# Kernel optimization log

Measured on AMD Instinct MI355X. Metric: run time of the kernel, lower is better.

## Reference

```python
import jax, jax.numpy as jnp
import numpy as np

B = 512      # parcels (batch)
P = 128      # pois per parcel
N = B * P    # poi nodes
E = 524288   # intra-parcel poi-poi edges
IN = 64
H = 128
OUT = 16
IMG = 2048
HEADS = 3


def seg_mean(x, seg, n):
    s = jax.ops.segment_sum(x, seg, num_segments=n)
    c = jax.ops.segment_sum(jnp.ones((x.shape[0],), x.dtype), seg, num_segments=n)
    return s / c[:, None]


def segment_softmax(e, seg, n):
    m = jax.ops.segment_max(e, seg, num_segments=n)
    ex = jnp.exp(e - m[seg])
    s = jax.ops.segment_sum(ex, seg, num_segments=n)
    return ex / s[seg]


def gcn_layer(x, src, dst, n, W, b):
    # symmetric-normalized GCN with self loops over an edge list
    deg = jax.ops.segment_sum(jnp.ones((src.shape[0],), x.dtype), dst, num_segments=n) + 1.0
    norm = jax.lax.rsqrt(deg)
    h = x * norm[:, None]
    agg = jax.ops.segment_sum(h[src], dst, num_segments=n) + h  # self loop
    return (agg * norm[:, None]) @ W + b


def gat(h_src_in, h_dst_in, src, dst, n_dst, W, al, ar, bias):
    # DGL-style GATConv (shared fc for src/dst), heads=HEADS
    hs = (h_src_in @ W).reshape(-1, HEADS, H)
    hd = (h_dst_in @ W).reshape(-1, HEADS, H)
    el = (hs * al).sum(-1)  # [Ns, heads]
    er = (hd * ar).sum(-1)  # [Nd, heads]
    e = jax.nn.leaky_relu(el[src] + er[dst], 0.2)  # [E, heads]
    alpha = segment_softmax(e, dst, n_dst)
    out = jax.ops.segment_sum(alpha[:, :, None] * hs[src], dst, num_segments=n_dst)
    return out + bias.reshape(HEADS, H)


def setup_inputs() -> dict:
    key = jax.random.key(0)
    ks = jax.random.split(key, 30)
    rng = np.random.default_rng(0)
    src = rng.integers(0, N, size=E)
    dst = (src // P) * P + rng.integers(0, P, size=E)  # intra-parcel edges
    edges = jnp.asarray(np.stack([src, dst]), dtype=jnp.int32)
    segment_ids = jnp.asarray(np.arange(N) // P, dtype=jnp.int32)
    s = 0.05
    n = lambda k, shp: jax.random.normal(k, shp, jnp.float32) * s
    return {
        "poi_x": jax.random.normal(ks[0], (N, IN), jnp.float32),
        "img_feat": jax.random.normal(ks[1], (B, IMG), jnp.float32),
        "edges": edges,
        "segment_ids": segment_ids,
        "T0": 0.98,
        # poi_encoder 2-layer GCN
        "W1": n(ks[2], (IN, H)), "b1": jnp.zeros((H,)),
        "W2": n(ks[3], (H, H)), "b2": jnp.zeros((H,)),
        # hrs_encoder.fc (ResNet backbone replaced by precomputed [B,2048] feats)
        "Whrs": n(ks[4], (IMG, H)), "bhrs": jnp.zeros((H,)),
        # proj_hrs / proj_poi
        "Wph": n(ks[5], (H, H)), "bph": jnp.zeros((H,)),
        "Wpp": n(ks[6], (H, H)), "bpp": jnp.zeros((H,)),
        # GATConv 'in' (poi -> parcel) and 'with' (parcel -> poi)
        "Wg_in": n(ks[7], (H, HEADS * H)), "al_in": n(ks[8], (HEADS, H)), "ar_in": n(ks[9], (HEADS, H)), "bg_in": jnp.zeros((HEADS * H,)),
        "Wg_w": n(ks[10], (H, HEADS * H)), "al_w": n(ks[11], (HEADS, H)), "ar_w": n(ks[12], (HEADS, H)), "bg_w": jnp.zeros((HEADS * H,)),
        # VanillaGCN (1 layer) on parcel similarity graph
        "Wh1": n(ks[13], (H, H)), "bh1": jnp.zeros((H,)),
        "Wp1": n(ks[14], (H, H)), "bp1": jnp.zeros((H,)),
        # final fc (4*hid -> out)
        "Wfc": n(ks[15], (4 * H, OUT)), "bfc": jnp.zeros((OUT,)),
    }


def reference(poi_x, img_feat, edges, segment_ids, T0,
              W1, b1, W2, b2, Whrs, bhrs, Wph, bph, Wpp, bpp,
              Wg_in, al_in, ar_in, bg_in, Wg_w, al_w, ar_w, bg_w,
              Wh1, bh1, Wp1, bp1, Wfc, bfc):
    src, dst = edges[0], edges[1]
    # encoders
    hrs = img_feat @ Whrs + bhrs                                   # [B,H]
    h1 = jax.nn.relu(gcn_layer(poi_x, src, dst, N, W1, b1))
    poi_node = gcn_layer(h1, src, dst, N, W2, b2)                  # [N,H]
    ori_poi = poi_node
    poi_pool = seg_mean(poi_node, segment_ids, B)                  # dgl.mean_nodes
    # parcel similarity
    med_fused = jnp.concatenate([hrs, poi_pool], axis=1)
    med_fused = med_fused / jnp.linalg.norm(med_fused, axis=1, keepdims=True)
    med = (med_fused @ med_fused.T + 1.0) / 2.0                    # [B,B]
    # UniSimGraph: threshold -> dense parcel graph -> 1-layer GCNs
    adj = jnp.maximum(jnp.where(med >= T0, 1.0, 0.0), jnp.eye(B, dtype=med.dtype))
    dinv = jax.lax.rsqrt(adj.sum(1))
    A = dinv[:, None] * adj * dinv[None, :]
    hrs_agg = A @ hrs @ Wh1 + bh1
    poi_agg = A @ poi_pool @ Wp1 + bp1
    # getHetGraph: bipartite GATs between pois and their parcel
    ph = hrs @ Wph + bph
    pp = ori_poi @ Wpp + bpp
    poi_idx = jnp.arange(N, dtype=segment_ids.dtype)
    poi2img = gat(pp, ph, poi_idx, segment_ids, B, Wg_in, al_in, ar_in, bg_in).mean(1)  # parcel out
    img2poi = gat(ph, pp, segment_ids, poi_idx, N, Wg_w, al_w, ar_w, bg_w).mean(1)      # poi out
    img2poi = seg_mean(img2poi, segment_ids, B)
    # MutualAgg concat order: [img2poi, poi2poi, poi2img, img2img]
    agg = jnp.concatenate([img2poi, poi_agg, poi2img, hrs_agg], axis=1)  # [B,4H]
    out = agg @ Wfc + bfc
    return out, med
```

## Files before the change

kernel.cpp:

```cpp
#include <hip/hip_runtime.h>
#include <stdint.h>

#define NN 65536
#define EE 524288
#define BB 512

typedef unsigned short u16;
typedef __attribute__((ext_vector_type(8))) short s8v;
typedef __attribute__((ext_vector_type(4))) float f32x4;

__device__ __forceinline__ u16 f2b(float f) {
  union { float f; uint32_t u; } a{f};
  uint32_t r = a.u + 0x7fff + ((a.u >> 16) & 1);
  return (u16)(r >> 16);
}
__device__ __forceinline__ float b2f(u16 v) {
  union { uint32_t u; float f; } a{(uint32_t)v << 16};
  return a.f;
}
__device__ __forceinline__ int swz128(int r, int c) { return r * 128 + (c ^ ((r & 7) << 3)); }
__device__ __forceinline__ int swz64(int r, int c) { return r * 64 + (c ^ ((r & 7) << 3)); }

__global__ void __launch_bounds__(256) k_prep_graph(
    const int* __restrict__ src, const int* __restrict__ dst, uint32_t* __restrict__ Sg,
    const float* __restrict__ W1, const float* __restrict__ W2,
    const float* __restrict__ Wg_in, const float* __restrict__ al_in,
    const float* __restrict__ ar_in, const float* __restrict__ Wpp,
    const float* __restrict__ bpp, u16* __restrict__ w1t, u16* __restrict__ w2t,
    float* __restrict__ wv, float* __restrict__ q, float* __restrict__ ch,
    const float* __restrict__ Wg_w, const float* __restrict__ Wfc,
    const float* __restrict__ bph, const float* __restrict__ bg_in,
    float* __restrict__ B0, float* __restrict__ Ch, float* __restrict__ D0,
    float* __restrict__ Evec, int* __restrict__ rowcnt) {
  int blk = blockIdx.x, t = threadIdx.x;
  if (blk < 2048) {
    int e = blk * 256 + t;
    int s = src[e] & 127, d = dst[e];
    atomicAdd(&Sg[((size_t)d * 128 + s) >> 2], 1u << ((s & 3) * 8));
  } else if (blk < 2144) {
    int i = (blk - 2048) * 256 + t;
    if (i < 8192) {
      int n = i >> 6, k = i & 63;
      w1t[i] = f2b(W1[k * 128 + n]);
    } else {
      int j = i - 8192;
      int n = j >> 7, k = j & 127;
      w2t[j] = f2b(W2[k * 128 + n]);
    }
  } else if (blk == 2144) {
    __shared__ float su[384];
    for (int i = t; i < 384; i += 256) {
      int h = i >> 7, k = i & 127;
      float s = 0.f, sw = 0.f;
#pragma unroll 4
      for (int c = 0; c < 128; ++c) {
        float g = Wg_in[k * 384 + h * 128 + c];
        s += g * al_in[h * 128 + c];
        sw += g * ar_in[h * 128 + c];
      }
      su[i] = s;
      wv[i] = sw;
    }
    __syncthreads();
    for (int i = t; i < 384; i += 256) {
      int h = i >> 7, j = i & 127;
      float s = 0.f;
#pragma unroll 4
      for (int k = 0; k < 128; ++k) s += Wpp[j * 128 + k] * su[h * 128 + k];
      q[i] = s;
    }
    if (t < 3) {
      float s = 0.f;
#pragma unroll 4
      for (int k = 0; k < 128; ++k) s += bpp[k] * su[t * 128 + k];
      ch[t] = s;
    }
  } else if (blk < 2153) {
    int bb = blk - 2145;
    __shared__ float sW[2048];
    for (int i = t; i < 2048; i += 256) sW[i] = Wfc[i];
    __syncthreads();
    int m = bb * 16 + (t >> 4), o = t & 15;
    const float* wr = Wg_w + (size_t)m * 384;
    float acc = 0.f;
#pragma unroll 4
    for (int j = 0; j < 128; ++j) {
      float g = (wr[j] + wr[128 + j] + wr[256 + j]) * (1.0f / 3.0f);
      acc += g * sW[j * 16 + o];
    }
    B0[m * 16 + o] = acc;
  } else if (blk < 2177) {
    int bb = blk - 2153;
    int h = bb >> 3, rc = bb & 7;
    __shared__ float sW[2048];
    for (int i = t; i < 2048; i += 256) sW[i] = Wfc[256 * 16 + i];
    __syncthreads();
    int m = rc * 16 + (t >> 4), o = t & 15;
    const float* wr = Wg_in + (size_t)m * 384 + h * 128;
    float acc = 0.f;
#pragma unroll 4
    for (int c = 0; c < 128; ++c) acc += wr[c] * sW[c * 16 + o];
    Ch[((size_t)h * 128 + m) * 16 + o] = acc;
  } else if (blk == 2177) {
    __shared__ float sD[2][128];
    int j = t & 127, half = t >> 7;
    int k0 = half * 64;
    float acc = 0.f;
#pragma unroll 4
    for (int k = k0; k < k0 + 64; ++k) {
      float g = (Wg_w[k * 384 + j] + Wg_w[k * 384 + 128 + j] + Wg_w[k * 384 + 256 + j]) *
                (1.0f / 3.0f);
      acc += bph[k] * g;
    }
    sD[half][j] = acc;
    __syncthreads();
    if (t < 128) D0[t] = sD[0][t] + sD[1][t];
  } else if (blk == 2178) {
    __shared__ float sE[2][128];
    int j = t & 127, half = t >> 7;
    int m0 = half * 64;
    float e = 0.f;
    for (int h = 0; h < 3; ++h) {
#pragma unroll 4
      for (int m = m0; m < m0 + 64; ++m) e += bpp[m] * Wg_in[m * 384 + h * 128 + j];
    }
    sE[half][j] = e;
    __syncthreads();
    if (t < 128) {
      float g0in = (bg_in[t] + bg_in[128 + t] + bg_in[256 + t]) * (1.0f / 3.0f);
      Evec[t] = (sE[0][t] + sE[1][t]) * (1.0f / 3.0f) + g0in;
    }
  } else {
    if (t < 256) {
      rowcnt[t] = 0;
      rowcnt[t + 256] = 0;
    }
  }
}

__global__ void __launch_bounds__(256) k_fold2(
    const float* __restrict__ Wph, const float* __restrict__ Wh1,
    const float* __restrict__ Wp1, const float* __restrict__ Wpp,
    const float* __restrict__ Wfc, const float* __restrict__ bfc,
    const float* __restrict__ bh1, const float* __restrict__ bp1,
    const float* __restrict__ bg_w, const float* __restrict__ B0,
    const float* __restrict__ Ch, const float* __restrict__ D0,
    const float* __restrict__ Evec, float* __restrict__ Afold,
    float* __restrict__ bias_out) {
  int blk = blockIdx.x, t = threadIdx.x;
  if (blk < 48) {
    int mat = blk >> 3, rc = blk & 7;
    __shared__ float sW[2048];
    if (mat == 0)
      for (int i = t; i < 2048; i += 256) sW[i] = B0[i];
    else if (mat == 1)
      for (int i = t; i < 2048; i += 256) sW[i] = Wfc[384 * 16 + i];
    else if (mat == 2)
      for (int i = t; i < 2048; i += 256) sW[i] = Wfc[128 * 16 + i];
    else
      for (int i = t; i < 2048; i += 256) sW[i] = Ch[(size_t)(mat - 3) * 2048 + i];
    __syncthreads();
    int k = rc * 16 + (t >> 4), o = t & 15;
    const float* L = (mat == 0) ? Wph : (mat == 1) ? Wh1 : (mat == 2) ? Wp1 : Wpp;
    float scale = (mat >= 3) ? (1.0f / 3.0f) : 1.0f;
    const float* lr = L + (size_t)k * 128;
    float acc = 0.f;
#pragma unroll 4
    for (int m = 0; m < 128; ++m) acc += lr[m] * sW[m * 16 + o];
    Afold[(size_t)mat * 2048 + k * 16 + o] = acc * scale;
  } else {
    __shared__ float sRed[16][16];
    int o = t & 15, chunk = t >> 4;
    int j0 = chunk * 8;
    float acc = 0.f;
#pragma unroll
    for (int jj = 0; jj < 8; ++jj) {
      int j = j0 + jj;
      float g0w = (bg_w[j] + bg_w[128 + j] + bg_w[256 + j]) * (1.0f / 3.0f);
      acc += (D0[j] + g0w) * Wfc[j * 16 + o];
      acc += bp1[j] * Wfc[(128 + j) * 16 + o];
      acc += Evec[j] * Wfc[(256 + j) * 16 + o];
      acc += bh1[j] * Wfc[(384 + j) * 16 + o];
    }
    sRed[o][chunk] = acc;
    __syncthreads();
    if (t < 16) {
      float a = bfc[t];
#pragma unroll
      for (int c = 0; c < 16; ++c) a += sRed[t][c];
      bias_out[t] = a;
    }
  }
}

__global__ void __launch_bounds__(1024) k_hrs(const float* __restrict__ img,
                                              const float* __restrict__ Whrs,
                                              const float* __restrict__ bhrs,
                                              const float* __restrict__ Wph,
                                              const float* __restrict__ bph,
                                              const float* __restrict__ wv,
                                              float* __restrict__ hrs, float* __restrict__ er) {
  __shared__ float sI[4096];
  __shared__ float sRed[8][128];
  __shared__ float sHrs[2][128];
  __shared__ float sPh[2][128];
  int r0 = blockIdx.x * 2;
  int t = threadIdx.x;
  const float4* gsrc = (const float4*)(img + (size_t)r0 * 2048);
  float4* ldst = (float4*)sI;
  if (t < 1024) ldst[t] = gsrc[t];
  __syncthreads();
  int c = t & 127, g = t >> 7;
  int row = g & 1, ks = g >> 1;
  const float* s = sI + row * 2048 + ks * 512;
  const float* W = Whrs + (size_t)(ks * 512) * 128 + c;
  float a0 = 0.f, a1 = 0.f, a2 = 0.f, a3 = 0.f;
  for (int k = 0; k < 512; k += 4) {
    a0 += s[k] * W[(size_t)k * 128];
    a1 += s[k + 1] * W[(size_t)(k + 1) * 128];
    a2 += s[k + 2] * W[(size_t)(k + 2) * 128];
    a3 += s[k + 3] * W[(size_t)(k + 3) * 128];
  }
  sRed[g][c] = (a0 + a1) + (a2 + a3);
  __syncthreads();
  if (t < 256) {
    int rr = t >> 7, cc = t & 127;
    float v = sRed[rr][cc] + sRed[rr + 2][cc] + sRed[rr + 4][cc] + sRed[rr + 6][cc] + bhrs[cc];
    hrs[(r0 + rr) * 128 + cc] = v;
    sHrs[rr][cc] = v;
  }
  __syncthreads();
  if (t < 256) {
    int rr = t >> 7, cc = t & 127;
    float acc = bph[cc];
#pragma unroll 4
    for (int k = 0; k < 128; ++k) acc += sHrs[rr][k] * Wph[k * 128 + cc];
    sPh[rr][cc] = acc;
  }
  __syncthreads();
  if (t < 6) {
    int rr = t / 3, h = t % 3;
    float s2 = 0.f;
#pragma unroll 4
    for (int k = 0; k < 128; ++k) s2 += sPh[rr][k] * wv[h * 128 + k];
    er[(r0 + rr) * 3 + h] = s2;
  }
}

__global__ void __launch_bounds__(1024) k_gcn_fused(
    const float* __restrict__ x, const float* __restrict__ b1, const float* __restrict__ b2,
    const uint8_t* __restrict__ Sg8, const float* __restrict__ q, const float* __restrict__ ch,
    const float* __restrict__ er, const float* __restrict__ hrs,
    const u16* __restrict__ w1t, const u16* __restrict__ w2t, float* __restrict__ poi_pool,
    float* __restrict__ pooled, u16* __restrict__ mfnb) {
  extern __shared__ char sm[];
  u16* sS = (u16*)sm;
  u16* sB2 = (u16*)(sm + 32768);
  u16* sPt = (u16*)(sm + 32768);
  u16* sXt = (u16*)(sm + 65536);
  u16* sAgg1 = (u16*)(sm + 81920);
  u16* sW1t = (u16*)(sm + 98304);
  float* sXrm = (float*)(sm + 114688);
  u16* sW2t = (u16*)(sm + 114688);
  u16* sAgg2 = (u16*)(sm + 65536);
  u16* sP = (u16*)sm;
  float* sNorm = (float*)(sm + 147968);
  float* sQ = (float*)(sm + 148480);
  float* sAl = (float*)(sm + 150016);
  float* sPool = (float*)(sm + 151552);
  float* sEr = (float*)(sm + 152064);
  float* sCh = (float*)(sm + 152080);

  int b = blockIdx.x, t = threadIdx.x;
  int base = b << 7;
  int l = t & 63, w = t >> 6;
  int wm = w & 7, wn = w >> 3;
  const uint8_t* Sgb = Sg8 + (size_t)base * 128;

  int rown = t >> 3, q8 = t & 7;
  uint4 cw = *(const uint4*)(Sgb + rown * 128 + q8 * 16);
  {
    uint32_t words[4] = {cw.x, cw.y, cw.z, cw.w};
    uint32_t bs = 0;
#pragma unroll
    for (int p = 0; p < 4; ++p)
      bs += (words[p] & 0xff) + ((words[p] >> 8) & 0xff) + ((words[p] >> 16) & 0xff) +
            (words[p] >> 24);
    bs += __shfl_xor((int)bs, 1);
    bs += __shfl_xor((int)bs, 2);
    bs += __shfl_xor((int)bs, 4);
    if ((t & 7) == 0) sNorm[rown] = rsqrtf((float)bs + 1.0f);
  }
  for (int i = t; i < 8192; i += 1024) {
    int s = i >> 6, f = i & 63;
    sXrm[s * 65 + f] = x[(size_t)(base + s) * 64 + f];
  }
  {
    int g = t;
    int n = g >> 3, blk = g & 7;
    *(uint4*)(sW1t + n * 64 + ((blk ^ (n & 7)) << 3)) = ((const uint4*)w1t)[g];
  }
  if (t < 384) sQ[t] = q[t];
  if (t < 3) {
    sEr[t] = er[b * 3 + t];
    sCh[t] = ch[t];
  }
  __syncthreads();

  {
    int r = rown;
    float nr = sNorm[r];
    int sw = (r & 7) << 3;
    uint32_t words[4] = {cw.x, cw.y, cw.z, cw.w};
#pragma unroll
    for (int qd = 0; qd < 4; ++qd) {
      uint32_t wd = words[qd];
#pragma unroll
      for (int p = 0; p < 4; p += 2) {
        int s0 = q8 * 16 + qd * 4 + p;
        float v0 = ((float)((wd >> (p * 8)) & 0xff) + (r == s0 ? 1.f : 0.f)) * nr * sNorm[s0];
        float v1 =
            ((float)((wd >> (p * 8 + 8)) & 0xff) + (r == s0 + 1 ? 1.f : 0.f)) * nr * sNorm[s0 + 1];
        uint32_t pk = (uint32_t)f2b(v0) | ((uint32_t)f2b(v1) << 16);
        *(uint32_t*)(sS + r * 128 + (s0 ^ sw)) = pk;
      }
    }
  }
  for (int i = t; i < 4096; i += 1024) {
    int f = i >> 6, s = (i & 63) * 2;
    float v0 = sXrm[s * 65 + f] * sNorm[s];
    float v1 = sXrm[(s + 1) * 65 + f] * sNorm[s + 1];
    uint32_t pk = (uint32_t)f2b(v0) | ((uint32_t)f2b(v1) << 16);
    *(uint32_t*)(sXt + (f * 128 + (s ^ ((f & 7) << 3)))) = pk;
  }
  __syncthreads();

  int mrow = wm * 16 + (l & 15);
  int kblk = (l >> 4) * 8;
  int rbase = wm * 16 + (l >> 4) * 4;

  {
    s8v a4[4];
#pragma unroll
    for (int ks = 0; ks < 4; ++ks) a4[ks] = *(const s8v*)(sS + swz128(mrow, ks * 32 + kblk));
#pragma unroll
    for (int j = 0; j < 2; ++j) {
      int nt = wn * 2 + j;
      f32x4 acc = {0.f, 0.f, 0.f, 0.f};
      int cg = nt * 16 + (l & 15);
#pragma unroll
      for (int ks = 0; ks < 4; ++ks)
        acc = __builtin_amdgcn_mfma_f32_16x16x32_bf16(
            a4[ks], *(const s8v*)(sXt + swz128(cg, ks * 32 + kblk)), acc, 0, 0, 0);
#pragma unroll
      for (int rg = 0; rg < 4; ++rg) sAgg1[swz64(rbase + rg, cg)] = f2b(acc[rg]);
    }
  }
  for (int g = t; g < 2048; g += 1024) {
    int n = g >> 4, blk = g & 15;
    *(uint4*)(sW2t + n * 128 + ((blk ^ (n & 7)) << 3)) = ((const uint4*)w2t)[g];
  }
  __syncthreads();

  {
    s8v a2[2];
#pragma unroll
    for (int ks = 0; ks < 2; ++ks) a2[ks] = *(const s8v*)(sAgg1 + swz64(mrow, ks * 32 + kblk));
#pragma unroll
    for (int j = 0; j < 4; ++j) {
      int nt = wn * 4 + j;
      int cg = nt * 16 + (l & 15);
      float bv = b1[cg];
      f32x4 acc = {bv, bv, bv, bv};
#pragma unroll
      for (int ks = 0; ks < 2; ++ks)
        acc = __builtin_amdgcn_mfma_f32_16x16x32_bf16(
            a2[ks], *(const s8v*)(sW1t + swz64(cg, ks * 32 + kblk)), acc, 0, 0, 0);
      u16 h0 = f2b(fmaxf(acc[0], 0.f)), h1v = f2b(fmaxf(acc[1], 0.f));
      u16 h2 = f2b(fmaxf(acc[2], 0.f)), h3 = f2b(fmaxf(acc[3], 0.f));
      uint2 pk;
      pk.x = (uint32_t)h0 | ((uint32_t)h1v << 16);
      pk.y = (uint32_t)h2 | ((uint32_t)h3 << 16);
      *(uint2*)(sB2 + swz128(cg, rbase)) = pk;
    }
  }
  __syncthreads();

  {
    s8v a4[4];
#pragma unroll
    for (int ks = 0; ks < 4; ++ks) a4[ks] = *(const s8v*)(sS + swz128(mrow, ks * 32 + kblk));
#pragma unroll
    for (int j = 0; j < 4; ++j) {
      int nt = wn * 4 + j;
      f32x4 acc = {0.f, 0.f, 0.f, 0.f};
      int cg = nt * 16 + (l & 15);
#pragma unroll
      for (int ks = 0; ks < 4; ++ks)
        acc = __builtin_amdgcn_mfma_f32_16x16x32_bf16(
            a4[ks], *(const s8v*)(sB2 + swz128(cg, ks * 32 + kblk)), acc, 0, 0, 0);
#pragma unroll
      for (int rg = 0; rg < 4; ++rg) sAgg2[swz128(rbase + rg, cg)] = f2b(acc[rg]);
    }
  }
  __syncthreads();

  {
    s8v a4[4];
#pragma unroll
    for (int ks = 0; ks < 4; ++ks) a4[ks] = *(const s8v*)(sAgg2 + swz128(mrow, ks * 32 + kblk));
#pragma unroll
    for (int j = 0; j < 4; ++j) {
      int nt = wn * 4 + j;
      int cg = nt * 16 + (l & 15);
      float bv = b2[cg];
      f32x4 acc = {bv, bv, bv, bv};
#pragma unroll
      for (int ks = 0; ks < 4; ++ks)
        acc = __builtin_amdgcn_mfma_f32_16x16x32_bf16(
            a4[ks], *(const s8v*)(sW2t + swz128(cg, ks * 32 + kblk)), acc, 0, 0, 0);
      u16 p0 = f2b(acc[0]), p1 = f2b(acc[1]), p2 = f2b(acc[2]), p3 = f2b(acc[3]);
#pragma unroll
      for (int rg = 0; rg < 4; ++rg)
        sP[swz128(rbase + rg, cg)] = (rg == 0) ? p0 : (rg == 1) ? p1 : (rg == 2) ? p2 : p3;
      uint2 pk;
      pk.x = (uint32_t)p0 | ((uint32_t)p1 << 16);
      pk.y = (uint32_t)p2 | ((uint32_t)p3 << 16);
      *(uint2*)(sPt + swz128(cg, rbase)) = pk;
    }
  }
  __syncthreads();

  if (t < 128) {
    int c = t;
    float s = 0.f;
    const u16* rowp = sPt + c * 128;
    int sw = (c & 7) << 3;
#pragma unroll
    for (int k8 = 0; k8 < 16; ++k8) {
      s8v v = *(const s8v*)(rowp + ((k8 * 8) ^ sw));
#pragma unroll
      for (int j = 0; j < 8; ++j) s += b2f((u16)v[j]);
    }
    sPool[c] = s;
    poi_pool[b * 128 + c] = s * (1.0f / 128.0f);
  }
  if (t < 384) {
    int r = t & 127, h = t >> 7;
    int sw = (r & 7) << 3;
    const u16* rowp = sP + r * 128;
    const float* qh = &sQ[h * 128];
    float d = 0.f;
#pragma unroll
    for (int k8 = 0; k8 < 16; ++k8) {
      int c8 = (k8 * 8) ^ sw;
      s8v v = *(const s8v*)(rowp + c8);
#pragma unroll
      for (int j = 0; j < 8; ++j) d += b2f((u16)v[j]) * qh[c8 + j];
    }
    float e = d + sCh[h] + sEr[h];
    sAl[h * 128 + r] = (e > 0.f) ? e : 0.2f * e;
  }
  __syncthreads();

  if (t < 192) {
    int h = t >> 6, ll = t & 63;
    float v0 = sAl[h * 128 + ll], v1 = sAl[h * 128 + 64 + ll];
    float m = fmaxf(v0, v1);
    for (int off = 32; off > 0; off >>= 1) m = fmaxf(m, __shfl_xor(m, off));
    float x0 = __expf(v0 - m), x1 = __expf(v1 - m);
    float s = x0 + x1;
    for (int off = 32; off > 0; off >>= 1) s += __shfl_xor(s, off);
    float inv = 1.0f / s;
    sAl[h * 128 + ll] = x0 * inv;
    sAl[h * 128 + 64 + ll] = x1 * inv;
  }
  __syncthreads();

  if (t < 384) {
    int hh = t >> 7, c = t & 127;
    int sw = (c & 7) << 3;
    const u16* rowp = sPt + c * 128;
    const float* al = &sAl[hh * 128];
    float s = 0.f;
#pragma unroll
    for (int k8 = 0; k8 < 16; ++k8) {
      int r8 = (k8 * 8) ^ sw;
      s8v v = *(const s8v*)(rowp + r8);
#pragma unroll
      for (int j = 0; j < 8; ++j) s += b2f((u16)v[j]) * al[r8 + j];
    }
    pooled[((size_t)b * 3 + hh) * 128 + c] = s;
  }
  __syncthreads();

  float hv = 0.f, pv = 0.f;
  if (t < 128) {
    hv = hrs[base + t];
    pv = sPool[t] * (1.0f / 128.0f);
    sQ[t] = hv * hv + pv * pv;
  }
  __syncthreads();
  if (t < 64) {
    float v = sQ[t] + sQ[t + 64];
    for (int off = 32; off > 0; off >>= 1) v += __shfl_xor(v, off);
    if (t == 0) sQ[0] = rsqrtf(v);
  }
  __syncthreads();
  if (t < 128) {
    float rn = sQ[0];
    mfnb[b * 256 + t] = f2b(hv * rn);
    mfnb[b * 256 + 128 + t] = f2b(pv * rn);
  }
}

__global__ void __launch_bounds__(256) k_med(const u16* __restrict__ mfnb,
                                             const float* __restrict__ T0p,
                                             float* __restrict__ med,
                                             int* __restrict__ rowcnt) {
  __shared__ u16 sA[32 * 256];
  __shared__ u16 sB[32 * 256];
  int bi = blockIdx.x >> 4, bj = blockIdx.x & 15;
  int t = threadIdx.x;
  const uint4* srcA = (const uint4*)(mfnb + (size_t)bi * 32 * 256);
  const uint4* srcB = (const uint4*)(mfnb + (size_t)bj * 32 * 256);
  for (int g = t; g < 1024; g += 256) {
    int r = g >> 5, blk = g & 31;
    int db = (blk & 24) | ((blk ^ (r & 7)) & 7);
    uint4 va = srcA[g];
    uint4 vb = srcB[g];
    *(uint4*)(sA + r * 256 + db * 8) = va;
    *(uint4*)(sB + r * 256 + db * 8) = vb;
  }
  __syncthreads();
  int l = t & 63, w = t >> 6;
  int wr = w >> 1, wc = w & 1;
  int arow = wr * 16 + (l & 15);
  int brow = wc * 16 + (l & 15);
  int kblk = (l >> 4) * 8;
  f32x4 acc = {0.f, 0.f, 0.f, 0.f};
#pragma unroll
  for (int ks = 0; ks < 8; ++ks) {
    int kc = ks * 32 + kblk;
    s8v a = *(const s8v*)(sA + arow * 256 + (kc ^ ((arow & 7) << 3)));
    s8v bb = *(const s8v*)(sB + brow * 256 + (kc ^ ((brow & 7) << 3)));
    acc = __builtin_amdgcn_mfma_f32_16x16x32_bf16(a, bb, acc, 0, 0, 0);
  }
  int row0 = bi * 32 + wr * 16 + (l >> 4) * 4;
  int col = bj * 32 + wc * 16 + (l & 15);
  float T0 = *T0p;
  int cnt4[4];
#pragma unroll
  for (int rg = 0; rg < 4; ++rg) {
    float m = (acc[rg] + 1.0f) * 0.5f;
    med[(size_t)(row0 + rg) * 512 + col] = m;
    cnt4[rg] = (m >= T0 || (row0 + rg) == col) ? 1 : 0;
  }
#pragma unroll
  for (int off = 1; off < 16; off <<= 1) {
#pragma unroll
    for (int rg = 0; rg < 4; ++rg) cnt4[rg] += __shfl_xor(cnt4[rg], off);
  }
  if ((l & 15) == 0) {
#pragma unroll
    for (int rg = 0; rg < 4; ++rg) atomicAdd(&rowcnt[row0 + rg], cnt4[rg]);
  }
}

__global__ void __launch_bounds__(256) k_epilogue(
    const float* __restrict__ med, const float* __restrict__ T0p,
    const int* __restrict__ rowcnt, const float* __restrict__ hrs,
    const float* __restrict__ pool, const float* __restrict__ pooled,
    const float* __restrict__ Afold, const float* __restrict__ bias_out,
    float* __restrict__ out) {
  __shared__ float sMedRow[512];
  __shared__ float sIn[6][128];
  __shared__ float sRed[16][16];
  __shared__ int sNbr[64];
  __shared__ float sDw[64];
  __shared__ int sNnz;
  int i = blockIdx.x, t = threadIdx.x;
  float T0 = *T0p;

  for (int j = t; j < 512; j += 256) sMedRow[j] = med[(size_t)i * 512 + j];
  if (t < 128) sIn[0][t] = hrs[i * 128 + t];
  for (int k = t; k < 384; k += 256) sIn[3 + (k >> 7)][k & 127] = pooled[(size_t)i * 384 + k];
  __syncthreads();

  if (t < 64) {
    int cnt = 0, flags = 0;
#pragma unroll
    for (int k = 0; k < 8; ++k) {
      int j = t * 8 + k;
      if (sMedRow[j] >= T0 || j == i) {
        flags |= 1 << k;
        ++cnt;
      }
    }
    int off = cnt;
    for (int d = 1; d < 64; d <<= 1) {
      int v = __shfl_up(off, d);
      if (t >= d) off += v;
    }
    off -= cnt;
    int pos = off;
#pragma unroll
    for (int k = 0; k < 8; ++k)
      if (flags & (1 << k)) {
        int j = t * 8 + k;
        if (pos < 64) {
          sNbr[pos] = j;
          sDw[pos] = rsqrtf((float)rowcnt[j]);
        }
        ++pos;
      }
    if (t == 63) sNnz = off + cnt;
  }
  __syncthreads();

  {
    int half = t >> 7, c = t & 127;
    float di = rsqrtf((float)rowcnt[i]);
    const float* srcm = half ? pool : hrs;
    float acc = 0.f;
    int nnz = sNnz;
    if (nnz <= 64) {
      for (int n = 0; n < nnz; ++n) acc += sDw[n] * srcm[sNbr[n] * 128 + c];
    } else {
      for (int j = 0; j < 512; ++j)
        if (sMedRow[j] >= T0 || j == i) acc += rsqrtf((float)rowcnt[j]) * srcm[j * 128 + c];
    }
    sIn[1 + half][c] = acc * di;
  }
  __syncthreads();

  {
    int o = t >> 4, chunk = t & 15;
    int c0 = chunk * 8;
    float acc = 0.f;
#pragma unroll
    for (int m = 0; m < 6; ++m) {
      const float* A = Afold + m * 2048;
      const float* xm = sIn[m];
#pragma unroll
      for (int k = 0; k < 8; ++k) acc += xm[c0 + k] * A[(c0 + k) * 16 + o];
    }
    sRed[o][chunk] = acc;
  }
  __syncthreads();
  if (t < 16) {
    float acc = bias_out[t];
#pragma unroll
    for (int j = 0; j < 16; ++j) acc += sRed[t][j];
    out[i * 16 + t] = acc;
  }
}

extern "C" void kernel_launch(void* const* d_in, const int* in_sizes, int n_in,
                              void* d_out, int out_size, void* d_ws, size_t ws_size,
                              hipStream_t stream) {
  const float* poi_x = (const float*)d_in[0];
  const float* img = (const float*)d_in[1];
  const int* edges = (const int*)d_in[2];
  const float* T0p = (const float*)d_in[4];
  const float* W1 = (const float*)d_in[5];
  const float* b1 = (const float*)d_in[6];
  const float* W2 = (const float*)d_in[7];
  const float* b2 = (const float*)d_in[8];
  const float* Whrs = (const float*)d_in[9];
  const float* bhrs = (const float*)d_in[10];
  const float* Wph = (const float*)d_in[11];
  const float* bph = (const float*)d_in[12];
  const float* Wpp = (const float*)d_in[13];
  const float* bpp = (const float*)d_in[14];
  const float* Wg_in = (const float*)d_in[15];
  const float* al_in = (const float*)d_in[16];
  const float* ar_in = (const float*)d_in[17];
  const float* bg_in = (const float*)d_in[18];
  const float* Wg_w = (const float*)d_in[19];
  const float* bg_w = (const float*)d_in[22];
  const float* Wh1 = (const float*)d_in[23];
  const float* bh1 = (const float*)d_in[24];
  const float* Wp1 = (const float*)d_in[25];
  const float* bp1 = (const float*)d_in[26];
  const float* Wfc = (const float*)d_in[27];
  const float* bfc = (const float*)d_in[28];

  const int* esrc = edges;
  const int* edst = edges + EE;

  char* ws = (char*)d_ws;
  size_t off = 0;
  auto alloc = [&](size_t nbytes) -> char* {
    char* p = ws + off;
    off += (nbytes + 255) & ~(size_t)255;
    return p;
  };
  uint8_t* Sg8 = (uint8_t*)alloc((size_t)NN * 128);
  u16* w1t = (u16*)alloc(8192 * 2);
  u16* w2t = (u16*)alloc(16384 * 2);
  float* hrs = (float*)alloc(512 * 128 * 4);
  float* er = (float*)alloc(512 * 3 * 4);
  float* wv = (float*)alloc(384 * 4);
  float* q = (float*)alloc(384 * 4);
  float* chv = (float*)alloc(16);
  float* B0 = (float*)alloc(2048 * 4);
  float* Chb = (float*)alloc(3 * 2048 * 4);
  float* D0 = (float*)alloc(128 * 4);
  float* Evec = (float*)alloc(128 * 4);
  float* Afold = (float*)alloc(6 * 2048 * 4);
  float* bias_out = (float*)alloc(16 * 4);
  float* pool = (float*)alloc(512 * 128 * 4);
  float* pooled = (float*)alloc((size_t)1536 * 128 * 4);
  u16* mfnb = (u16*)alloc(512 * 256 * 2);
  int* rowcnt = (int*)alloc(512 * 4);

  float* out = (float*)d_out;
  float* med = out + 512 * 16;

  hipMemsetAsync(Sg8, 0, (size_t)NN * 128, stream);

  size_t dynf = 152096;
  hipFuncSetAttribute((const void*)k_gcn_fused, hipFuncAttributeMaxDynamicSharedMemorySize,
                      (int)dynf);

  k_prep_graph<<<2180, 256, 0, stream>>>(esrc, edst, (uint32_t*)Sg8, W1, W2, Wg_in, al_in,
                                         ar_in, Wpp, bpp, w1t, w2t, wv, q, chv, Wg_w, Wfc, bph,
                                         bg_in, B0, Chb, D0, Evec, rowcnt);
  k_fold2<<<49, 256, 0, stream>>>(Wph, Wh1, Wp1, Wpp, Wfc, bfc, bh1, bp1, bg_w, B0, Chb, D0,
                                  Evec, Afold, bias_out);
  k_hrs<<<256, 1024, 0, stream>>>(img, Whrs, bhrs, Wph, bph, wv, hrs, er);
  k_gcn_fused<<<512, 1024, dynf, stream>>>(poi_x, b1, b2, Sg8, q, chv, er, hrs, w1t, w2t, pool,
                                           pooled, mfnb);
  k_med<<<256, 256, 0, stream>>>(mfnb, T0p, med, rowcnt);
  k_epilogue<<<512, 256, 0, stream>>>(med, T0p, rowcnt, hrs, pool, pooled, Afold, bias_out,
                                      out);

  (void)in_sizes; (void)n_in; (void)out_size; (void)ws_size;
}
```

Before: 141.6 us.

## Merge fold and hrs kernels; split pooling/attention reductions across more threads

```diff
diff --git a/kernel.cpp b/kernel.cpp
--- a/kernel.cpp
+++ b/kernel.cpp
@@ -138,112 +138,109 @@
   }
 }
 
-__global__ void __launch_bounds__(256) k_fold2(
-    const float* __restrict__ Wph, const float* __restrict__ Wh1,
-    const float* __restrict__ Wp1, const float* __restrict__ Wpp,
-    const float* __restrict__ Wfc, const float* __restrict__ bfc,
-    const float* __restrict__ bh1, const float* __restrict__ bp1,
-    const float* __restrict__ bg_w, const float* __restrict__ B0,
-    const float* __restrict__ Ch, const float* __restrict__ D0,
-    const float* __restrict__ Evec, float* __restrict__ Afold,
-    float* __restrict__ bias_out) {
-  int blk = blockIdx.x, t = threadIdx.x;
-  if (blk < 48) {
-    int mat = blk >> 3, rc = blk & 7;
-    __shared__ float sW[2048];
-    if (mat == 0)
-      for (int i = t; i < 2048; i += 256) sW[i] = B0[i];
-    else if (mat == 1)
-      for (int i = t; i < 2048; i += 256) sW[i] = Wfc[384 * 16 + i];
-    else if (mat == 2)
-      for (int i = t; i < 2048; i += 256) sW[i] = Wfc[128 * 16 + i];
-    else
-      for (int i = t; i < 2048; i += 256) sW[i] = Ch[(size_t)(mat - 3) * 2048 + i];
-    __syncthreads();
-    int k = rc * 16 + (t >> 4), o = t & 15;
-    const float* L = (mat == 0) ? Wph : (mat == 1) ? Wh1 : (mat == 2) ? Wp1 : Wpp;
-    float scale = (mat >= 3) ? (1.0f / 3.0f) : 1.0f;
-    const float* lr = L + (size_t)k * 128;
-    float acc = 0.f;
-#pragma unroll 4
-    for (int m = 0; m < 128; ++m) acc += lr[m] * sW[m * 16 + o];
-    Afold[(size_t)mat * 2048 + k * 16 + o] = acc * scale;
-  } else {
-    __shared__ float sRed[16][16];
-    int o = t & 15, chunk = t >> 4;
-    int j0 = chunk * 8;
-    float acc = 0.f;
-#pragma unroll
-    for (int jj = 0; jj < 8; ++jj) {
-      int j = j0 + jj;
-      float g0w = (bg_w[j] + bg_w[128 + j] + bg_w[256 + j]) * (1.0f / 3.0f);
-      acc += (D0[j] + g0w) * Wfc[j * 16 + o];
-      acc += bp1[j] * Wfc[(128 + j) * 16 + o];
-      acc += Evec[j] * Wfc[(256 + j) * 16 + o];
-      acc += bh1[j] * Wfc[(384 + j) * 16 + o];
-    }
-    sRed[o][chunk] = acc;
-    __syncthreads();
-    if (t < 16) {
-      float a = bfc[t];
-#pragma unroll
-      for (int c = 0; c < 16; ++c) a += sRed[t][c];
-      bias_out[t] = a;
-    }
-  }
-}
-
-__global__ void __launch_bounds__(1024) k_hrs(const float* __restrict__ img,
-                                              const float* __restrict__ Whrs,
-                                              const float* __restrict__ bhrs,
-                                              const float* __restrict__ Wph,
-                                              const float* __restrict__ bph,
-                                              const float* __restrict__ wv,
-                                              float* __restrict__ hrs, float* __restrict__ er) {
+__global__ void __launch_bounds__(1024) k_hrsfold(
+    const float* __restrict__ img, const float* __restrict__ Whrs,
+    const float* __restrict__ bhrs, const float* __restrict__ Wph,
+    const float* __restrict__ bph, const float* __restrict__ wv, float* __restrict__ hrs,
+    float* __restrict__ er, const float* __restrict__ Wh1, const float* __restrict__ Wp1,
+    const float* __restrict__ Wpp, const float* __restrict__ Wfc,
+    const float* __restrict__ bfc, const float* __restrict__ bh1,
+    const float* __restrict__ bp1, const float* __restrict__ bg_w,
+    const float* __restrict__ B0, const float* __restrict__ Ch, const float* __restrict__ D0,
+    const float* __restrict__ Evec, float* __restrict__ Afold, float* __restrict__ bias_out) {
   __shared__ float sI[4096];
   __shared__ float sRed[8][128];
   __shared__ float sHrs[2][128];
   __shared__ float sPh[2][128];
-  int r0 = blockIdx.x * 2;
+  __shared__ float sW[2048];
+  __shared__ float sRed2[16][16];
   int t = threadIdx.x;
-  const float4* gsrc = (const float4*)(img + (size_t)r0 * 2048);
-  float4* ldst = (float4*)sI;
-  if (t < 1024) ldst[t] = gsrc[t];
-  __syncthreads();
-  int c = t & 127, g = t >> 7;
-  int row = g & 1, ks = g >> 1;
-  const float* s = sI + row * 2048 + ks * 512;
-  const float* W = Whrs + (size_t)(ks * 512) * 128 + c;
-  float a0 = 0.f, a1 = 0.f, a2 = 0.f, a3 = 0.f;
-  for (int k = 0; k < 512; k += 4) {
-    a0 += s[k] * W[(size_t)k * 128];
-    a1 += s[k + 1] * W[(size_t)(k + 1) * 128];
-    a2 += s[k + 2] * W[(size_t)(k + 2) * 128];
-    a3 += s[k + 3] * W[(size_t)(k + 3) * 128];
-  }
-  sRed[g][c] = (a0 + a1) + (a2 + a3);
-  __syncthreads();
-  if (t < 256) {
-    int rr = t >> 7, cc = t & 127;
-    float v = sRed[rr][cc] + sRed[rr + 2][cc] + sRed[rr + 4][cc] + sRed[rr + 6][cc] + bhrs[cc];
-    hrs[(r0 + rr) * 128 + cc] = v;
-    sHrs[rr][cc] = v;
-  }
-  __syncthreads();
-  if (t < 256) {
-    int rr = t >> 7, cc = t & 127;
-    float acc = bph[cc];
-#pragma unroll 4
-    for (int k = 0; k < 128; ++k) acc += sHrs[rr][k] * Wph[k * 128 + cc];
-    sPh[rr][cc] = acc;
-  }
-  __syncthreads();
-  if (t < 6) {
-    int rr = t / 3, h = t % 3;
-    float s2 = 0.f;
-#pragma unroll 4
-    for (int k = 0; k < 128; ++k) s2 += sPh[rr][k] * wv[h * 128 + k];
-    er[(r0 + rr) * 3 + h] = s2;
+  if (blockIdx.x < 256) {
+    int r0 = blockIdx.x * 2;
+    const float4* gsrc = (const float4*)(img + (size_t)r0 * 2048);
+    float4* ldst = (float4*)sI;
+    ldst[t] = gsrc[t];
+    __syncthreads();
+    int c = t & 127, g = t >> 7;
+    int row = g & 1, ks = g >> 1;
+    const float* s = sI + row * 2048 + ks * 512;
+    const float* W = Whrs + (size_t)(ks * 512) * 128 + c;
+    float a0 = 0.f, a1 = 0.f, a2 = 0.f, a3 = 0.f;
+    for (int k = 0; k < 512; k += 4) {
+      a0 += s[k] * W[(size_t)k * 128];
+      a1 += s[k + 1] * W[(size_t)(k + 1) * 128];
+      a2 += s[k + 2] * W[(size_t)(k + 2) * 128];
+      a3 += s[k + 3] * W[(size_t)(k + 3) * 128];
+    }
+    sRed[g][c] = (a0 + a1) + (a2 + a3);
+    __syncthreads();
+    if (t < 256) {
+      int rr = t >> 7, cc = t & 127;
+      float v = sRed[rr][cc] + sRed[rr + 2][cc] + sRed[rr + 4][cc] + sRed[rr + 6][cc] + bhrs[cc];
+      hrs[(r0 + rr) * 128 + cc] = v;
+      sHrs[rr][cc] = v;
+    }
+    __syncthreads();
+    if (t < 256) {
+      int rr = t >> 7, cc = t & 127;
+      float acc = bph[cc];
+#pragma unroll 4
+      for (int k = 0; k < 128; ++k) acc += sHrs[rr][k] * Wph[k * 128 + cc];
+      sPh[rr][cc] = acc;
+    }
+    __syncthreads();
+    if (t < 6) {
+      int rr = t / 3, h = t % 3;
+      float s2 = 0.f;
+#pragma unroll 4
+      for (int k = 0; k < 128; ++k) s2 += sPh[rr][k] * wv[h * 128 + k];
+      er[(r0 + rr) * 3 + h] = s2;
+    }
+  } else if (blockIdx.x < 304) {
+    int blk = blockIdx.x - 256;
+    int mat = blk >> 3, rc = blk & 7;
+    if (mat == 0)
+      for (int i = t; i < 2048; i += 1024) sW[i] = B0[i];
+    else if (mat == 1)
+      for (int i = t; i < 2048; i += 1024) sW[i] = Wfc[384 * 16 + i];
+    else if (mat == 2)
+      for (int i = t; i < 2048; i += 1024) sW[i] = Wfc[128 * 16 + i];
+    else
+      for (int i = t; i < 2048; i += 1024) sW[i] = Ch[(size_t)(mat - 3) * 2048 + i];
+    __syncthreads();
+    if (t < 256) {
+      int k = rc * 16 + (t >> 4), o = t & 15;
+      const float* L = (mat == 0) ? Wph : (mat == 1) ? Wh1 : (mat == 2) ? Wp1 : Wpp;
+      float scale = (mat >= 3) ? (1.0f / 3.0f) : 1.0f;
+      const float* lr = L + (size_t)k * 128;
+      float acc = 0.f;
+#pragma unroll 4
+      for (int m = 0; m < 128; ++m) acc += lr[m] * sW[m * 16 + o];
+      Afold[(size_t)mat * 2048 + k * 16 + o] = acc * scale;
+    }
+  } else {
+    if (t < 256) {
+      int o = t & 15, chunk = t >> 4;
+      int j0 = chunk * 8;
+      float acc = 0.f;
+#pragma unroll
+      for (int jj = 0; jj < 8; ++jj) {
+        int j = j0 + jj;
+        float g0w = (bg_w[j] + bg_w[128 + j] + bg_w[256 + j]) * (1.0f / 3.0f);
+        acc += (D0[j] + g0w) * Wfc[j * 16 + o];
+        acc += bp1[j] * Wfc[(128 + j) * 16 + o];
+        acc += Evec[j] * Wfc[(256 + j) * 16 + o];
+        acc += bh1[j] * Wfc[(384 + j) * 16 + o];
+      }
+      sRed2[o][chunk] = acc;
+    }
+    __syncthreads();
+    if (t < 16) {
+      float a = bfc[t];
+#pragma unroll
+      for (int c = 0; c < 16; ++c) a += sRed2[t][c];
+      bias_out[t] = a;
+    }
   }
 }
 
@@ -270,6 +267,8 @@
   float* sPool = (float*)(sm + 151552);
   float* sEr = (float*)(sm + 152064);
   float* sCh = (float*)(sm + 152080);
+  float* sElp = (float*)(sm + 152320);
+  float* sPoolp = (float*)(sm + 155392);
 
   int b = blockIdx.x, t = threadIdx.x;
   int base = b << 7;
@@ -296,9 +295,8 @@
     sXrm[s * 65 + f] = x[(size_t)(base + s) * 64 + f];
   }
   {
-    int g = t;
-    int n = g >> 3, blk = g & 7;
-    *(uint4*)(sW1t + n * 64 + ((blk ^ (n & 7)) << 3)) = ((const uint4*)w1t)[g];
+    int n = t >> 3, blk = t & 7;
+    *(uint4*)(sW1t + n * 64 + ((blk ^ (n & 7)) << 3)) = ((const uint4*)w1t)[t];
   }
   if (t < 384) sQ[t] = q[t];
   if (t < 3) {
@@ -431,34 +429,46 @@
   }
   __syncthreads();
 
-  if (t < 128) {
-    int c = t;
+  if (t < 256) {
+    int c = t & 127, kh = t >> 7;
     float s = 0.f;
     const u16* rowp = sPt + c * 128;
     int sw = (c & 7) << 3;
 #pragma unroll
-    for (int k8 = 0; k8 < 16; ++k8) {
+    for (int k8 = kh * 8; k8 < kh * 8 + 8; ++k8) {
       s8v v = *(const s8v*)(rowp + ((k8 * 8) ^ sw));
 #pragma unroll
       for (int j = 0; j < 8; ++j) s += b2f((u16)v[j]);
     }
-    sPool[c] = s;
-    poi_pool[b * 128 + c] = s * (1.0f / 128.0f);
-  }
-  if (t < 384) {
-    int r = t & 127, h = t >> 7;
+    sPoolp[kh * 128 + c] = s;
+  } else {
+    int task = t - 256;
+    int r = task & 127, hk = task >> 7;
+    int h = hk >> 1, kh = hk & 1;
     int sw = (r & 7) << 3;
     const u16* rowp = sP + r * 128;
     const float* qh = &sQ[h * 128];
     float d = 0.f;
 #pragma unroll
-    for (int k8 = 0; k8 < 16; ++k8) {
+    for (int k8 = kh * 8; k8 < kh * 8 + 8; ++k8) {
       int c8 = (k8 * 8) ^ sw;
       s8v v = *(const s8v*)(rowp + c8);
 #pragma unroll
       for (int j = 0; j < 8; ++j) d += b2f((u16)v[j]) * qh[c8 + j];
     }
-    float e = d + sCh[h] + sEr[h];
+    sElp[hk * 128 + r] = d;
+  }
+  __syncthreads();
+
+  if (t < 128) {
+    float s = sPoolp[t] + sPoolp[128 + t];
+    sPool[t] = s;
+    poi_pool[b * 128 + t] = s * (1.0f / 128.0f);
+  }
+  if (t >= 512 && t < 896) {
+    int tt = t - 512;
+    int h = tt >> 7, r = tt & 127;
+    float e = sElp[h * 256 + r] + sElp[h * 256 + 128 + r] + sCh[h] + sEr[h];
     sAl[h * 128 + r] = (e > 0.f) ? e : 0.2f * e;
   }
   __syncthreads();
@@ -477,20 +487,27 @@
   }
   __syncthreads();
 
-  if (t < 384) {
-    int hh = t >> 7, c = t & 127;
+  if (t < 768) {
+    int c = t & 127, hk = t >> 7;
+    int hh = hk >> 1, kh = hk & 1;
     int sw = (c & 7) << 3;
     const u16* rowp = sPt + c * 128;
     const float* al = &sAl[hh * 128];
     float s = 0.f;
 #pragma unroll
-    for (int k8 = 0; k8 < 16; ++k8) {
+    for (int k8 = kh * 8; k8 < kh * 8 + 8; ++k8) {
       int r8 = (k8 * 8) ^ sw;
       s8v v = *(const s8v*)(rowp + r8);
 #pragma unroll
       for (int j = 0; j < 8; ++j) s += b2f((u16)v[j]) * al[r8 + j];
     }
-    pooled[((size_t)b * 3 + hh) * 128 + c] = s;
+    sElp[hk * 128 + c] = s;
+  }
+  __syncthreads();
+
+  if (t < 384) {
+    int hh = t >> 7, c = t & 127;
+    pooled[((size_t)b * 3 + hh) * 128 + c] = sElp[hh * 256 + c] + sElp[hh * 256 + 128 + c];
   }
   __syncthreads();
 
@@ -720,16 +737,16 @@
 
   hipMemsetAsync(Sg8, 0, (size_t)NN * 128, stream);
 
-  size_t dynf = 152096;
+  size_t dynf = 156416;
   hipFuncSetAttribute((const void*)k_gcn_fused, hipFuncAttributeMaxDynamicSharedMemorySize,
                       (int)dynf);
 
   k_prep_graph<<<2180, 256, 0, stream>>>(esrc, edst, (uint32_t*)Sg8, W1, W2, Wg_in, al_in,
                                          ar_in, Wpp, bpp, w1t, w2t, wv, q, chv, Wg_w, Wfc, bph,
                                          bg_in, B0, Chb, D0, Evec, rowcnt);
-  k_fold2<<<49, 256, 0, stream>>>(Wph, Wh1, Wp1, Wpp, Wfc, bfc, bh1, bp1, bg_w, B0, Chb, D0,
-                                  Evec, Afold, bias_out);
-  k_hrs<<<256, 1024, 0, stream>>>(img, Whrs, bhrs, Wph, bph, wv, hrs, er);
+  k_hrsfold<<<305, 1024, 0, stream>>>(img, Whrs, bhrs, Wph, bph, wv, hrs, er, Wh1, Wp1, Wpp,
+                                      Wfc, bfc, bh1, bp1, bg_w, B0, Chb, D0, Evec, Afold,
+                                      bias_out);
   k_gcn_fused<<<512, 1024, dynf, stream>>>(poi_x, b1, b2, Sg8, q, chv, er, hrs, w1t, w2t, pool,
                                            pooled, mfnb);
   k_med<<<256, 256, 0, stream>>>(mfnb, T0p, med, rowcnt);
```

New measurement: 137.3 us. -3.0%, faster.
